# Optimization experiments

Hardware: AMD Instinct MI355X
Metric: run time of the kernel (lower is better)

## Reference

```python
import jax, jax.numpy as jnp
import numpy as np

NUM_HEADS = 8
T = 8  # hardcoded temporal dim in the original forward
MD = 3  # max_displacement -> 7x7 window
EPS = 1e-12  # F.normalize eps


def l2_normalize(x, axis):
    n = jnp.sqrt(jnp.sum(x * x, axis=axis, keepdims=True))
    return x / jnp.maximum(n, EPS)


def correlation_7x7(q, k):
    # q, k: [B, C, H, W]; FlowNet-style correlation, kernel_size=1, max_disp=3.
    # out[b, u, v, h, w] = sum_c q[b,c,h,w] * k[b,c,h+u-3,w+v-3] (zero padded)
    B, C, H, W = q.shape
    kp = jnp.pad(k, ((0, 0), (0, 0), (MD, MD), (MD, MD)))
    outs = []
    for dy in range(2 * MD + 1):
        for dx in range(2 * MD + 1):
            ks = kp[:, :, dy:dy + H, dx:dx + W]
            outs.append(jnp.sum(q * ks, axis=1))  # [B, H, W]
    corr = jnp.stack(outs, axis=1)  # [B, 49, H, W]
    return corr.reshape(B, 2 * MD + 1, 2 * MD + 1, H, W)


def setup_inputs() -> dict:
    key = jax.random.key(0)
    ks = jax.random.split(key, 6)
    B, N, C = 8, 8192, 256
    hd = C // NUM_HEADS
    std = 0.02
    return {
        "x": jax.random.normal(ks[0], (B, N, C), dtype=jnp.float32),
        "w_qk": jax.random.normal(ks[1], (2 * C, C), dtype=jnp.float32) * std,
        "w_corr": jax.random.normal(ks[2], (hd, 49), dtype=jnp.float32) * std,
        "b_corr": jnp.zeros((hd,), dtype=jnp.float32),
        "w_proj": jax.random.normal(ks[3], (C, C), dtype=jnp.float32) * std,
        "b_proj": jnp.zeros((C,), dtype=jnp.float32),
    }


def reference(x, w_qk, w_corr, b_corr, w_proj, b_proj):
    B, N, C = x.shape
    nh = NUM_HEADS
    hd = C // nh
    H = int(np.sqrt(N // T))
    W = H

    # qk projection (no bias): [B, N, 2C] -> q, k each [B, nh, N, hd]
    qk = jnp.einsum('bnc,dc->bnd', x, w_qk)
    qk = qk.reshape(B, N, 2, nh, hd).transpose(2, 0, 3, 1, 4)
    q, k = qk[0], qk[1]

    # 'b n (t h w) d -> (b n) t d h w'
    q = q.reshape(B * nh, T, H, W, hd).transpose(0, 1, 4, 2, 3)
    k = k.reshape(B * nh, T, H, W, hd).transpose(0, 1, 4, 2, 3)

    # temporal postfix: k[t+1], last frame repeated
    k_post = jnp.concatenate([k[:, 1:], k[:, -1:]], axis=1)

    qp = q.reshape(B * nh * T, hd, H, W)
    kp = k_post.reshape(B * nh * T, hd, H, W)
    qp = l2_normalize(qp, axis=1)
    kp = l2_normalize(kp, axis=1)

    corr = correlation_7x7(qp, kp)  # [(B nh T), 7, 7, H, W]
    # 'b u v h w -> b (h w) (u v)'
    corr = corr.transpose(0, 3, 4, 1, 2).reshape(B * nh * T, H * W, 49)

    v = jnp.einsum('bpk,dk->bpd', corr, w_corr) + b_corr  # [(B nh T), HW, hd]

    # '(b n t) (h w) d -> b n (t h w) d' then 'b h n d -> b n (h d)'
    out = v.reshape(B, nh, T * H * W, hd).transpose(0, 2, 1, 3).reshape(B, N, C)
    out = jnp.einsum('bnc,dc->bnd', out, w_proj) + b_proj
    return out
```

## Files before the change

kernel.cpp:

```cpp
#include <hip/hip_runtime.h>

typedef _Float16 half8 __attribute__((ext_vector_type(8)));
typedef _Float16 half2v __attribute__((ext_vector_type(2)));
typedef float float4v __attribute__((ext_vector_type(4)));

__device__ __forceinline__ float dot2acc(unsigned a, unsigned b, float c) {
#if __has_builtin(__builtin_amdgcn_fdot2)
  return __builtin_amdgcn_fdot2(__builtin_bit_cast(half2v, a), __builtin_bit_cast(half2v, b), c, false);
#else
  half2v ha = __builtin_bit_cast(half2v, a);
  half2v hb = __builtin_bit_cast(half2v, b);
  c += (float)ha[0] * (float)hb[0];
  c += (float)ha[1] * (float)hb[1];
  return c;
#endif
}
__device__ __forceinline__ unsigned pack2(float a, float b) {
  half2v h;
  h[0] = (_Float16)a;
  h[1] = (_Float16)b;
  return __builtin_bit_cast(unsigned, h);
}
__device__ __forceinline__ void gload_lds16(const void* g, void* l) {
  __builtin_amdgcn_global_load_lds((const __attribute__((address_space(1))) unsigned*)g,
                                   (__attribute__((address_space(3))) unsigned*)l, 16, 0, 0);
}
__device__ __forceinline__ void sbar0() { __builtin_amdgcn_sched_barrier(0); }
#define WAITVM(n) asm volatile("s_waitcnt vmcnt(" #n ")" ::: "memory")
#define WAITLGKM asm volatile("s_waitcnt lgkmcnt(0)" ::: "memory")

__device__ __forceinline__ void cvt_store8(_Float16* dst, float4 a, float4 b) {
  half8 h;
  h[0] = (_Float16)a.x; h[1] = (_Float16)a.y; h[2] = (_Float16)a.z; h[3] = (_Float16)a.w;
  h[4] = (_Float16)b.x; h[5] = (_Float16)b.y; h[6] = (_Float16)b.z; h[7] = (_Float16)b.w;
  *(half8*)dst = h;
}

__global__ void cvt_w(const float4* __restrict__ wqk, const float4* __restrict__ wpj,
                      ushort4* __restrict__ wqk16, ushort4* __restrict__ wpj16) {
  int b = blockIdx.x;
  const float4* s;
  ushort4* d;
  int i;
  if (b < 128) { s = wqk; d = wqk16; i = b * 256 + threadIdx.x; }
  else { s = wpj; d = wpj16; i = (b - 128) * 256 + threadIdx.x; }
  float4 v = s[i];
  _Float16 a = (_Float16)v.x, bb = (_Float16)v.y, c = (_Float16)v.z, e = (_Float16)v.w;
  ushort4 o;
  o.x = __builtin_bit_cast(unsigned short, a);
  o.y = __builtin_bit_cast(unsigned short, bb);
  o.z = __builtin_bit_cast(unsigned short, c);
  o.w = __builtin_bit_cast(unsigned short, e);
  d[i] = o;
}

__global__ __launch_bounds__(512, 4)
void gemm_qk(const float* __restrict__ X, const _Float16* __restrict__ Bw,
             _Float16* __restrict__ qo, _Float16* __restrict__ ko) {
  __shared__ _Float16 Ash[2][4096];
  __shared__ _Float16 Bsh[2][8192];
  const int tid = threadIdx.x;
  const int lane = tid & 63, w = tid >> 6;
  const int wm = w >> 2, wn = w & 3;
  const int ml = lane & 15, qd = lane >> 4;
  const int bid = blockIdx.x;
  const int yb = ((bid >> 4) << 3) | (bid & 7);
  const int xb = (bid >> 3) & 1;
  const int m0 = yb * 128, n0 = xb * 256;

  float4v acc[4][4];
  float4v z = {0.f, 0.f, 0.f, 0.f};
#pragma unroll
  for (int i = 0; i < 4; ++i)
#pragma unroll
    for (int j = 0; j < 4; ++j) acc[i][j] = z;

  const float* Xp = X + (size_t)m0 * 256;
  const _Float16* Bp = Bw + (size_t)n0 * 256;
  const int ar = tid >> 2, aj = tid & 3;
  const int ajx = aj ^ ((ar >> 1) & 3);
  const int rB0 = tid >> 2, jB0 = (tid & 3) ^ ((rB0 >> 1) & 3);
  const int rB1 = rB0 + 128, jB1 = (tid & 3) ^ ((rB1 >> 1) & 3);

  float4 xs[2][2];
  gload_lds16(Bp + rB0 * 256 + jB0 * 8, &Bsh[0][(size_t)(w * 64) * 8]);
  gload_lds16(Bp + rB1 * 256 + jB1 * 8, &Bsh[0][(size_t)(512 + w * 64) * 8]);
  sbar0();
  xs[0][0] = *(const float4*)(Xp + (size_t)ar * 256 + ajx * 8);
  xs[0][1] = *(const float4*)(Xp + (size_t)ar * 256 + ajx * 8 + 4);
  sbar0();
  xs[1][0] = *(const float4*)(Xp + (size_t)ar * 256 + 32 + ajx * 8);
  xs[1][1] = *(const float4*)(Xp + (size_t)ar * 256 + 32 + ajx * 8 + 4);
  WAITVM(2);
  sbar0();
  cvt_store8(&Ash[0][ar * 32 + aj * 8], xs[0][0], xs[0][1]);
  WAITLGKM;
  sbar0();
  __builtin_amdgcn_s_barrier();
  sbar0();

#pragma unroll
  for (int kt = 0; kt < 8; ++kt) {
    const int cur = kt & 1, nbuf = cur ^ 1;
    const int kB = (kt + 1 < 8 ? kt + 1 : 7) * 32;
    const int kX = (kt + 2 < 8 ? kt + 2 : 7) * 32;
    gload_lds16(Bp + rB0 * 256 + kB + jB0 * 8, &Bsh[nbuf][(size_t)(w * 64) * 8]);
    gload_lds16(Bp + rB1 * 256 + kB + jB1 * 8, &Bsh[nbuf][(size_t)(512 + w * 64) * 8]);
    sbar0();
    xs[kt & 1][0] = *(const float4*)(Xp + (size_t)ar * 256 + kX + ajx * 8);
    xs[kt & 1][1] = *(const float4*)(Xp + (size_t)ar * 256 + kX + ajx * 8 + 4);
    half8 af[4], bf[4];
#pragma unroll
    for (int im = 0; im < 4; ++im) {
      int rr = wm * 64 + im * 16 + ml;
      af[im] = *(const half8*)(&Ash[cur][rr * 32 + (qd ^ ((rr >> 1) & 3)) * 8]);
      int rc = wn * 64 + im * 16 + ml;
      bf[im] = *(const half8*)(&Bsh[cur][rc * 32 + (qd ^ ((rc >> 1) & 3)) * 8]);
    }
#pragma unroll
    for (int im = 0; im < 4; ++im)
#pragma unroll
      for (int in = 0; in < 4; ++in)
        acc[im][in] = __builtin_amdgcn_mfma_f32_16x16x32_f16(bf[in], af[im], acc[im][in], 0, 0, 0);
    WAITVM(2);
    sbar0();
    cvt_store8(&Ash[nbuf][ar * 32 + aj * 8], xs[(kt + 1) & 1][0], xs[(kt + 1) & 1][1]);
    WAITLGKM;
    sbar0();
    __builtin_amdgcn_s_barrier();
    sbar0();
  }

#pragma unroll
  for (int im = 0; im < 4; ++im) {
    int rowr = m0 + wm * 64 + im * 16 + ml;
    int b = rowr >> 13, n = rowr & 8191;
    int t = n >> 10, yx = n & 1023;
#pragma unroll
    for (int hh = 0; hh < 2; ++hh) {
      float ss = 0.f;
#pragma unroll
      for (int ii = 0; ii < 2; ++ii) {
        int in = hh * 2 + ii;
#pragma unroll
        for (int r = 0; r < 4; ++r) ss += acc[im][in][r] * acc[im][in][r];
      }
      ss += __shfl_xor(ss, 16);
      ss += __shfl_xor(ss, 32);
      float sc = 1.f / fmaxf(sqrtf(ss), 1e-12f);
#pragma unroll
      for (int ii = 0; ii < 2; ++ii) {
        int in = hh * 2 + ii;
        int col = n0 + wn * 64 + in * 16 + qd * 4;
        int s = col >> 8, h = (col >> 5) & 7, j = col & 31;
        _Float16* dst = s ? ko : qo;
        int p = b * 64 + h * 8 + t;
        uint2 pk;
        pk.x = pack2(acc[im][in][0] * sc, acc[im][in][1] * sc);
        pk.y = pack2(acc[im][in][2] * sc, acc[im][in][3] * sc);
        *(uint2*)(dst + ((size_t)p * 1024 + yx) * 32 + j) = pk;
      }
    }
  }
}

__global__ __launch_bounds__(256, 4)
void corr_kernel(const _Float16* __restrict__ q16, const _Float16* __restrict__ k16,
                 const float* __restrict__ wcorr, const float* __restrict__ bcorr,
                 _Float16* __restrict__ outp) {
  __shared__ uint4 smem[2304];
  __shared__ uint4 wcs[256];

  const int tid = threadIdx.x;
  const int bx = blockIdx.x;
  const int p = bx >> 2, tile = bx & 3;
  const int y0 = (tile >> 1) * 16, x0 = (tile & 1) * 16;
  const int b = p >> 6, h = (p >> 3) & 7, t = p & 7;
  const int pk = (t < 7) ? p + 1 : p;
  const int ty = tid >> 4, tx = tid & 15;

  _Float16* wch = (_Float16*)wcs;
  for (int idx = tid; idx < 2048; idx += 256) {
    int d = idx >> 6, kk = idx & 63;
    float v = (kk < 49) ? wcorr[d * 49 + kk] : (kk == 49 ? bcorr[d] : 0.f);
    wch[idx] = (_Float16)v;
  }

  const _Float16* kbase = k16 + (size_t)pk * 32768;
#pragma unroll
  for (int i = 0; i < 8; ++i) {
    int g = tid + i * 256;
    if (g < 1936) {
      int vec = g >> 2, part = g & 3;
      int ky = vec / 22, kx = vec - ky * 22;
      int gy = y0 + ky - 3, gx = x0 + kx - 3;
      uint4 val = make_uint4(0u, 0u, 0u, 0u);
      if (gy >= 0 && gy < 32 && gx >= 0 && gx < 32)
        val = *(const uint4*)(kbase + ((size_t)gy * 32 + gx) * 32 + part * 8);
      int slot = (vec << 2) | (part ^ (vec & 3) ^ ((vec >> 2) & 3));
      smem[slot] = val;
    }
  }

  const _Float16* qptr = q16 + (size_t)p * 32768 + ((size_t)(y0 + ty) * 32 + (x0 + tx)) * 32;
  uint4 qv[4];
#pragma unroll
  for (int i = 0; i < 4; ++i) qv[i] = *(const uint4*)(qptr + i * 8);
  unsigned* qu = (unsigned*)qv;
  __syncthreads();

  float corr[49];
#pragma unroll
  for (int dy = 0; dy < 7; ++dy) {
#pragma unroll
    for (int dx = 0; dx < 7; ++dx) {
      int vec = (ty + dy) * 22 + (tx + dx);
      int base = vec << 2;
      int sw = (vec & 3) ^ ((vec >> 2) & 3);
      float c = 0.f;
#pragma unroll
      for (int pq = 0; pq < 4; ++pq) {
        uint4 kk = smem[base | (pq ^ sw)];
        const unsigned* ku = (const unsigned*)&kk;
#pragma unroll
        for (int e = 0; e < 4; ++e) c = dot2acc(qu[pq * 4 + e], ku[e], c);
      }
      corr[dy * 7 + dx] = c;
    }
  }
  __syncthreads();

#pragma unroll
  for (int i = 0; i < 8; ++i) {
    uint4 val;
    unsigned* vu = (unsigned*)&val;
#pragma unroll
    for (int e = 0; e < 4; ++e) {
      int idx = i * 8 + e * 2;
      half2v hh;
      hh[0] = (_Float16)(idx < 49 ? corr[idx] : (idx == 49 ? 1.f : 0.f));
      hh[1] = (_Float16)(idx + 1 < 49 ? corr[idx + 1] : (idx + 1 == 49 ? 1.f : 0.f));
      vu[e] = __builtin_bit_cast(unsigned, hh);
    }
    smem[tid * 9 + i] = val;
  }
  __syncthreads();

  _Float16* corrm = (_Float16*)smem;
  const int lane = tid & 63, w = tid >> 6;
  const int ml = lane & 15, qd = lane >> 4;
  float4v vacc[4][2];
  float4v z = {0.f, 0.f, 0.f, 0.f};
#pragma unroll
  for (int im = 0; im < 4; ++im) { vacc[im][0] = z; vacc[im][1] = z; }
#pragma unroll
  for (int ks = 0; ks < 2; ++ks) {
    half8 bfrag[2];
#pragma unroll
    for (int nt = 0; nt < 2; ++nt)
      bfrag[nt] = *(const half8*)(wch + (nt * 16 + ml) * 64 + ks * 32 + qd * 8);
#pragma unroll
    for (int im = 0; im < 4; ++im) {
      half8 afrag = *(const half8*)(corrm + (w * 64 + im * 16 + ml) * 72 + ks * 32 + qd * 8);
#pragma unroll
      for (int nt = 0; nt < 2; ++nt)
        vacc[im][nt] = __builtin_amdgcn_mfma_f32_16x16x32_f16(afrag, bfrag[nt], vacc[im][nt], 0, 0, 0);
    }
  }

#pragma unroll
  for (int im = 0; im < 4; ++im) {
#pragma unroll
    for (int nt = 0; nt < 2; ++nt) {
      int d = nt * 16 + ml;
#pragma unroll
      for (int r = 0; r < 4; ++r) {
        int pos = w * 64 + im * 16 + qd * 4 + r;
        int py = pos >> 4, px = pos & 15;
        int n = t * 1024 + (y0 + py) * 32 + (x0 + px);
        outp[(((size_t)b * 8192 + n) << 8) + h * 32 + d] = (_Float16)vacc[im][nt][r];
      }
    }
  }
}

__global__ __launch_bounds__(512, 4)
void gemm_proj(const _Float16* __restrict__ A, const _Float16* __restrict__ Bw,
               const float* __restrict__ bp, float* __restrict__ out) {
  __shared__ _Float16 Ash[2][4096];
  __shared__ _Float16 Bsh[2][8192];
  const int tid = threadIdx.x;
  const int lane = tid & 63, w = tid >> 6;
  const int wm = w >> 2, wn = w & 3;
  const int ml = lane & 15, qd = lane >> 4;
  const int m0 = blockIdx.x * 128;

  float4v acc[4][4];
  float4v z = {0.f, 0.f, 0.f, 0.f};
#pragma unroll
  for (int i = 0; i < 4; ++i)
#pragma unroll
    for (int j = 0; j < 4; ++j) acc[i][j] = z;

  const _Float16* Ap = A + (size_t)m0 * 256;
  const _Float16* Bp = Bw;
  const int ar = tid >> 2, aj = tid & 3;
  const int ajx = aj ^ ((ar >> 1) & 3);
  const int rB0 = tid >> 2, jB0 = (tid & 3) ^ ((rB0 >> 1) & 3);
  const int rB1 = rB0 + 128, jB1 = (tid & 3) ^ ((rB1 >> 1) & 3);

  uint4 as[2];
  gload_lds16(Bp + rB0 * 256 + jB0 * 8, &Bsh[0][(size_t)(w * 64) * 8]);
  gload_lds16(Bp + rB1 * 256 + jB1 * 8, &Bsh[0][(size_t)(512 + w * 64) * 8]);
  sbar0();
  as[0] = *(const uint4*)(Ap + (size_t)ar * 256 + ajx * 8);
  sbar0();
  as[1] = *(const uint4*)(Ap + (size_t)ar * 256 + 32 + ajx * 8);
  WAITVM(1);
  sbar0();
  *(uint4*)(&Ash[0][ar * 32 + aj * 8]) = as[0];
  WAITLGKM;
  sbar0();
  __builtin_amdgcn_s_barrier();
  sbar0();

#pragma unroll
  for (int kt = 0; kt < 8; ++kt) {
    const int cur = kt & 1, nbuf = cur ^ 1;
    const int kB = (kt + 1 < 8 ? kt + 1 : 7) * 32;
    const int kA = (kt + 2 < 8 ? kt + 2 : 7) * 32;
    gload_lds16(Bp + rB0 * 256 + kB + jB0 * 8, &Bsh[nbuf][(size_t)(w * 64) * 8]);
    gload_lds16(Bp + rB1 * 256 + kB + jB1 * 8, &Bsh[nbuf][(size_t)(512 + w * 64) * 8]);
    sbar0();
    as[kt & 1] = *(const uint4*)(Ap + (size_t)ar * 256 + kA + ajx * 8);
    half8 af[4], bf[4];
#pragma unroll
    for (int im = 0; im < 4; ++im) {
      int rr = wm * 64 + im * 16 + ml;
      af[im] = *(const half8*)(&Ash[cur][rr * 32 + (qd ^ ((rr >> 1) & 3)) * 8]);
      int rc = wn * 64 + im * 16 + ml;
      bf[im] = *(const half8*)(&Bsh[cur][rc * 32 + (qd ^ ((rc >> 1) & 3)) * 8]);
    }
#pragma unroll
    for (int im = 0; im < 4; ++im)
#pragma unroll
      for (int in = 0; in < 4; ++in)
        acc[im][in] = __builtin_amdgcn_mfma_f32_16x16x32_f16(bf[in], af[im], acc[im][in], 0, 0, 0);
    WAITVM(1);
    sbar0();
    *(uint4*)(&Ash[nbuf][ar * 32 + aj * 8]) = as[(kt + 1) & 1];
    WAITLGKM;
    sbar0();
    __builtin_amdgcn_s_barrier();
    sbar0();
  }

#pragma unroll
  for (int im = 0; im < 4; ++im) {
    int rowr = m0 + wm * 64 + im * 16 + ml;
#pragma unroll
    for (int in = 0; in < 4; ++in) {
      int col = wn * 64 + in * 16 + qd * 4;
      float4 bb = *(const float4*)(bp + col);
      float4 o;
      o.x = acc[im][in][0] + bb.x;
      o.y = acc[im][in][1] + bb.y;
      o.z = acc[im][in][2] + bb.z;
      o.w = acc[im][in][3] + bb.w;
      *(float4*)(out + (size_t)rowr * 256 + col) = o;
    }
  }
}

extern "C" void kernel_launch(void* const* d_in, const int* in_sizes, int n_in,
                              void* d_out, int out_size, void* d_ws, size_t ws_size,
                              hipStream_t stream) {
  const float* x      = (const float*)d_in[0];
  const float* w_qk   = (const float*)d_in[1];
  const float* w_corr = (const float*)d_in[2];
  const float* b_corr = (const float*)d_in[3];
  const float* w_proj = (const float*)d_in[4];
  const float* b_proj = (const float*)d_in[5];
  float* out = (float*)d_out;

  char* ws = (char*)d_ws;
  _Float16* q16   = (_Float16*)(ws + 33554432);
  _Float16* k16   = (_Float16*)(ws + 67108864);
  _Float16* op16  = (_Float16*)(ws + 100663296);
  _Float16* wqk16 = (_Float16*)(ws + 134217728);
  _Float16* wpj16 = (_Float16*)(ws + 134479872);

  cvt_w<<<192, 256, 0, stream>>>((const float4*)w_qk, (const float4*)w_proj,
                                 (ushort4*)wqk16, (ushort4*)wpj16);
  gemm_qk<<<1024, 512, 0, stream>>>(x, wqk16, q16, k16);
  corr_kernel<<<2048, 256, 0, stream>>>(q16, k16, w_corr, b_corr, op16);
  gemm_proj<<<512, 512, 0, stream>>>(op16, wpj16, b_proj, out);
}
```

Measured before the change: 217.0 us.

## Replace direct global-to-LDS weight loads with register-staged prefetch in GEMMs

Both GEMM kernels stop using global_load_lds for the weight tile. They now load the B tile into registers two k-steps ahead, the same way A is staged, and write it to LDS with ds_write after the MFMAs. The last iterations skip redundant prefetches and the final barrier. The explicit vmcnt waits and the 4-block occupancy hint in launch_bounds are removed. This costs more VGPRs and LDS writes, and may change occupancy and how well memory latency overlaps with compute.

```diff
diff --git a/kernel.cpp b/kernel.cpp
--- a/kernel.cpp
+++ b/kernel.cpp
@@ -21,12 +21,7 @@
   h[1] = (_Float16)b;
   return __builtin_bit_cast(unsigned, h);
 }
-__device__ __forceinline__ void gload_lds16(const void* g, void* l) {
-  __builtin_amdgcn_global_load_lds((const __attribute__((address_space(1))) unsigned*)g,
-                                   (__attribute__((address_space(3))) unsigned*)l, 16, 0, 0);
-}
 __device__ __forceinline__ void sbar0() { __builtin_amdgcn_sched_barrier(0); }
-#define WAITVM(n) asm volatile("s_waitcnt vmcnt(" #n ")" ::: "memory")
 #define WAITLGKM asm volatile("s_waitcnt lgkmcnt(0)" ::: "memory")
 
 __device__ __forceinline__ void cvt_store8(_Float16* dst, float4 a, float4 b) {
@@ -54,7 +49,7 @@
   d[i] = o;
 }
 
-__global__ __launch_bounds__(512, 4)
+__global__ __launch_bounds__(512)
 void gemm_qk(const float* __restrict__ X, const _Float16* __restrict__ Bw,
              _Float16* __restrict__ qo, _Float16* __restrict__ ko) {
   __shared__ _Float16 Ash[2][4096];
@@ -83,17 +78,19 @@
   const int rB1 = rB0 + 128, jB1 = (tid & 3) ^ ((rB1 >> 1) & 3);
 
   float4 xs[2][2];
-  gload_lds16(Bp + rB0 * 256 + jB0 * 8, &Bsh[0][(size_t)(w * 64) * 8]);
-  gload_lds16(Bp + rB1 * 256 + jB1 * 8, &Bsh[0][(size_t)(512 + w * 64) * 8]);
-  sbar0();
+  uint4 bs[2][2];
+
   xs[0][0] = *(const float4*)(Xp + (size_t)ar * 256 + ajx * 8);
   xs[0][1] = *(const float4*)(Xp + (size_t)ar * 256 + ajx * 8 + 4);
-  sbar0();
+  bs[0][0] = *(const uint4*)(Bp + (size_t)rB0 * 256 + jB0 * 8);
+  bs[0][1] = *(const uint4*)(Bp + (size_t)rB1 * 256 + jB1 * 8);
+  cvt_store8(&Ash[0][ar * 32 + aj * 8], xs[0][0], xs[0][1]);
+  *(uint4*)(&Bsh[0][tid * 8]) = bs[0][0];
+  *(uint4*)(&Bsh[0][(tid + 512) * 8]) = bs[0][1];
   xs[1][0] = *(const float4*)(Xp + (size_t)ar * 256 + 32 + ajx * 8);
   xs[1][1] = *(const float4*)(Xp + (size_t)ar * 256 + 32 + ajx * 8 + 4);
-  WAITVM(2);
-  sbar0();
-  cvt_store8(&Ash[0][ar * 32 + aj * 8], xs[0][0], xs[0][1]);
+  bs[1][0] = *(const uint4*)(Bp + (size_t)rB0 * 256 + 32 + jB0 * 8);
+  bs[1][1] = *(const uint4*)(Bp + (size_t)rB1 * 256 + 32 + jB1 * 8);
   WAITLGKM;
   sbar0();
   __builtin_amdgcn_s_barrier();
@@ -102,13 +99,14 @@
 #pragma unroll
   for (int kt = 0; kt < 8; ++kt) {
     const int cur = kt & 1, nbuf = cur ^ 1;
-    const int kB = (kt + 1 < 8 ? kt + 1 : 7) * 32;
-    const int kX = (kt + 2 < 8 ? kt + 2 : 7) * 32;
-    gload_lds16(Bp + rB0 * 256 + kB + jB0 * 8, &Bsh[nbuf][(size_t)(w * 64) * 8]);
-    gload_lds16(Bp + rB1 * 256 + kB + jB1 * 8, &Bsh[nbuf][(size_t)(512 + w * 64) * 8]);
-    sbar0();
-    xs[kt & 1][0] = *(const float4*)(Xp + (size_t)ar * 256 + kX + ajx * 8);
-    xs[kt & 1][1] = *(const float4*)(Xp + (size_t)ar * 256 + kX + ajx * 8 + 4);
+    if (kt < 6) {
+      const int kX = (kt + 2) * 32;
+      xs[kt & 1][0] = *(const float4*)(Xp + (size_t)ar * 256 + kX + ajx * 8);
+      xs[kt & 1][1] = *(const float4*)(Xp + (size_t)ar * 256 + kX + ajx * 8 + 4);
+      bs[kt & 1][0] = *(const uint4*)(Bp + (size_t)rB0 * 256 + kX + jB0 * 8);
+      bs[kt & 1][1] = *(const uint4*)(Bp + (size_t)rB1 * 256 + kX + jB1 * 8);
+      sbar0();
+    }
     half8 af[4], bf[4];
 #pragma unroll
     for (int im = 0; im < 4; ++im) {
@@ -122,13 +120,15 @@
 #pragma unroll
       for (int in = 0; in < 4; ++in)
         acc[im][in] = __builtin_amdgcn_mfma_f32_16x16x32_f16(bf[in], af[im], acc[im][in], 0, 0, 0);
-    WAITVM(2);
-    sbar0();
-    cvt_store8(&Ash[nbuf][ar * 32 + aj * 8], xs[(kt + 1) & 1][0], xs[(kt + 1) & 1][1]);
-    WAITLGKM;
-    sbar0();
-    __builtin_amdgcn_s_barrier();
-    sbar0();
+    if (kt < 7) {
+      cvt_store8(&Ash[nbuf][ar * 32 + aj * 8], xs[(kt + 1) & 1][0], xs[(kt + 1) & 1][1]);
+      *(uint4*)(&Bsh[nbuf][tid * 8]) = bs[(kt + 1) & 1][0];
+      *(uint4*)(&Bsh[nbuf][(tid + 512) * 8]) = bs[(kt + 1) & 1][1];
+      WAITLGKM;
+      sbar0();
+      __builtin_amdgcn_s_barrier();
+      sbar0();
+    }
   }
 
 #pragma unroll
@@ -284,7 +284,7 @@
   }
 }
 
-__global__ __launch_bounds__(512, 4)
+__global__ __launch_bounds__(512)
 void gemm_proj(const _Float16* __restrict__ A, const _Float16* __restrict__ Bw,
                const float* __restrict__ bp, float* __restrict__ out) {
   __shared__ _Float16 Ash[2][4096];
@@ -310,15 +310,17 @@
   const int rB1 = rB0 + 128, jB1 = (tid & 3) ^ ((rB1 >> 1) & 3);
 
   uint4 as[2];
-  gload_lds16(Bp + rB0 * 256 + jB0 * 8, &Bsh[0][(size_t)(w * 64) * 8]);
-  gload_lds16(Bp + rB1 * 256 + jB1 * 8, &Bsh[0][(size_t)(512 + w * 64) * 8]);
-  sbar0();
+  uint4 bs[2][2];
+
   as[0] = *(const uint4*)(Ap + (size_t)ar * 256 + ajx * 8);
-  sbar0();
+  bs[0][0] = *(const uint4*)(Bp + (size_t)rB0 * 256 + jB0 * 8);
+  bs[0][1] = *(const uint4*)(Bp + (size_t)rB1 * 256 + jB1 * 8);
+  *(uint4*)(&Ash[0][ar * 32 + aj * 8]) = as[0];
+  *(uint4*)(&Bsh[0][tid * 8]) = bs[0][0];
+  *(uint4*)(&Bsh[0][(tid + 512) * 8]) = bs[0][1];
   as[1] = *(const uint4*)(Ap + (size_t)ar * 256 + 32 + ajx * 8);
-  WAITVM(1);
-  sbar0();
-  *(uint4*)(&Ash[0][ar * 32 + aj * 8]) = as[0];
+  bs[1][0] = *(const uint4*)(Bp + (size_t)rB0 * 256 + 32 + jB0 * 8);
+  bs[1][1] = *(const uint4*)(Bp + (size_t)rB1 * 256 + 32 + jB1 * 8);
   WAITLGKM;
   sbar0();
   __builtin_amdgcn_s_barrier();
@@ -327,12 +329,13 @@
 #pragma unroll
   for (int kt = 0; kt < 8; ++kt) {
     const int cur = kt & 1, nbuf = cur ^ 1;
-    const int kB = (kt + 1 < 8 ? kt + 1 : 7) * 32;
-    const int kA = (kt + 2 < 8 ? kt + 2 : 7) * 32;
-    gload_lds16(Bp + rB0 * 256 + kB + jB0 * 8, &Bsh[nbuf][(size_t)(w * 64) * 8]);
-    gload_lds16(Bp + rB1 * 256 + kB + jB1 * 8, &Bsh[nbuf][(size_t)(512 + w * 64) * 8]);
-    sbar0();
-    as[kt & 1] = *(const uint4*)(Ap + (size_t)ar * 256 + kA + ajx * 8);
+    if (kt < 6) {
+      const int kX = (kt + 2) * 32;
+      as[kt & 1] = *(const uint4*)(Ap + (size_t)ar * 256 + kX + ajx * 8);
+      bs[kt & 1][0] = *(const uint4*)(Bp + (size_t)rB0 * 256 + kX + jB0 * 8);
+      bs[kt & 1][1] = *(const uint4*)(Bp + (size_t)rB1 * 256 + kX + jB1 * 8);
+      sbar0();
+    }
     half8 af[4], bf[4];
 #pragma unroll
     for (int im = 0; im < 4; ++im) {
@@ -346,13 +349,15 @@
 #pragma unroll
       for (int in = 0; in < 4; ++in)
         acc[im][in] = __builtin_amdgcn_mfma_f32_16x16x32_f16(bf[in], af[im], acc[im][in], 0, 0, 0);
-    WAITVM(1);
-    sbar0();
-    *(uint4*)(&Ash[nbuf][ar * 32 + aj * 8]) = as[(kt + 1) & 1];
-    WAITLGKM;
-    sbar0();
-    __builtin_amdgcn_s_barrier();
-    sbar0();
+    if (kt < 7) {
+      *(uint4*)(&Ash[nbuf][ar * 32 + aj * 8]) = as[(kt + 1) & 1];
+      *(uint4*)(&Bsh[nbuf][tid * 8]) = bs[(kt + 1) & 1][0];
+      *(uint4*)(&Bsh[nbuf][(tid + 512) * 8]) = bs[(kt + 1) & 1][1];
+      WAITLGKM;
+      sbar0();
+      __builtin_amdgcn_s_barrier();
+      sbar0();
+    }
   }
 
 #pragma unroll
```

Measured after the change: 209.3 us. 3.5% less time.
